# Performance work log

Measured on AMD Instinct MI355X. Metric: run time of the kernel, lower is better.

## Reference

```python
import jax, jax.numpy as jnp
import numpy as np

B, L, H, NL = 32, 1024, 4, 2
D_BERT, D_PHY, D_ACC = 1024, 7, 2
C_IN = D_BERT + D_PHY + D_ACC
D = 32
K = 20
N = B * L
E = N * K


def setup_inputs() -> dict:
    key = jax.random.key(0)
    ks = jax.random.split(key, 10)
    return {
        "protbert": jax.random.normal(ks[0], (B, 1, L, D_BERT), jnp.float32),
        "phychem": jax.random.normal(ks[1], (B, 1, L, D_PHY), jnp.float32),
        "resacc": jax.random.normal(ks[2], (B, 1, L, D_ACC), jnp.float32),
        "edge_feat": jax.random.normal(ks[3], (E, 2), jnp.float32),
        "src_idx": jax.random.randint(ks[4], (E,), 0, N, jnp.int32),
        "dst_idx": (jnp.arange(E, dtype=jnp.int32) % N),  # every node gets exactly K in-edges
        "conv_w": jax.random.normal(ks[5], (D, C_IN, 7), jnp.float32) * 0.02,
        "conv_b": jnp.zeros((D,), jnp.float32),
        "bn_gamma": jnp.ones((D,), jnp.float32),
        "bn_beta": jnp.zeros((D,), jnp.float32),
        "bn_mean": jnp.zeros((D,), jnp.float32),
        "bn_var": jnp.ones((D,), jnp.float32),
        "fc_w": jax.random.normal(ks[6], (NL, H, D, D), jnp.float32) * 0.1,
        "attn_w": jax.random.normal(ks[7], (NL, H, 2 * D + 2), jnp.float32) * 0.1,
        "fc_edge_w": jax.random.normal(ks[8], (NL, H, D, 2), jnp.float32) * 0.1,
        "fc_eatt_w": jax.random.normal(ks[9], (NL, H, 2, 2), jnp.float32) * 0.1,
    }


def _leaky(x):
    return jnp.where(x >= 0, x, 0.01 * x)


def _seg_softmax(e, dst, n):
    # softmax over incoming edges of each destination node (DGL mailbox softmax)
    m = jax.ops.segment_max(e, dst, num_segments=n)
    ex = jnp.exp(e - m[dst])
    s = jax.ops.segment_sum(ex, dst, num_segments=n)
    return ex / s[dst]


def reference(protbert, phychem, resacc, edge_feat, src_idx, dst_idx,
              conv_w, conv_b, bn_gamma, bn_beta, bn_mean, bn_var,
              fc_w, attn_w, fc_edge_w, fc_eatt_w):
    # --- Conv1d + LeakyReLU + BatchNorm1d (eval) encoder ---
    x = jnp.concatenate([protbert, phychem, resacc], axis=3)[:, 0]  # (B,L,C_IN)
    x = jnp.transpose(x, (0, 2, 1))  # (B,C_IN,L)
    x = jax.lax.conv_general_dilated(x, conv_w, (1,), [(3, 3)],
                                     dimension_numbers=("NCH", "OIH", "NCH"))
    x = _leaky(x + conv_b[None, :, None])
    scale = (bn_gamma / jnp.sqrt(bn_var + 1e-5))[None, :, None]
    x = (x - bn_mean[None, :, None]) * scale + bn_beta[None, :, None]
    feats = jnp.transpose(x, (0, 2, 1))  # (B,L,D)

    # --- stacked multi-head EGRET layers on flattened batched graph ---
    h = feats.reshape(N, D)
    alpha = None
    for l in range(NL):
        z = jnp.einsum("nd,hod->nho", h, fc_w[l])                    # (N,H,D)
        ex_t = jnp.einsum("ef,hgf->ehg", edge_feat, fc_eatt_w[l])    # (E,H,2) transformed edge feats for attn
        ez = jnp.einsum("ef,hof->eho", edge_feat, fc_edge_w[l])      # (E,H,D) edge messages
        a_src = attn_w[l][:, :D]
        a_dst = attn_w[l][:, D:2 * D]
        a_e = attn_w[l][:, 2 * D:]
        s_src = jnp.einsum("nhd,hd->nh", z, a_src)                   # node-level partial scores
        s_dst = jnp.einsum("nhd,hd->nh", z, a_dst)
        e = _leaky(s_src[src_idx] + s_dst[dst_idx]
                   + jnp.einsum("ehg,hg->eh", ex_t, a_e))            # (E,H)
        alpha = _seg_softmax(e, dst_idx, N)                          # (E,H)
        msg = alpha[:, :, None] * (z[src_idx] + ez)                  # attn on node+edge messages
        h = jax.ops.segment_sum(msg, dst_idx, num_segments=N).mean(axis=1)  # merge='avg'

    feats2 = h.reshape(B, L, D)
    out = jnp.concatenate([feats2, feats], axis=2)  # (B,L,2D)
    return out, alpha
```

## Files before the change

kernel.cpp:

```cpp
#include <hip/hip_runtime.h>
#include <hip/hip_bf16.h>
#include <cstdint>

#define B_   32
#define L_   1024
#define H_   4
#define NL_  2
#define D_   32
#define K_   20
#define N_   (B_ * L_)
#define E_   (N_ * K_)

typedef __attribute__((ext_vector_type(8))) __bf16 bf16x8;
typedef __attribute__((ext_vector_type(4))) float  f32x4;
typedef __attribute__((ext_vector_type(2))) float  f32x2;
typedef __attribute__((ext_vector_type(4))) int    i32x4;

static __device__ __forceinline__ float leaky1(float x) { return x >= 0.f ? x : 0.01f * x; }

static __device__ __forceinline__ bf16x8 cvt8(f32x4 lo, f32x4 hi) {
    bf16x8 r;
    r[0] = (__bf16)lo[0]; r[1] = (__bf16)lo[1]; r[2] = (__bf16)lo[2]; r[3] = (__bf16)lo[3];
    r[4] = (__bf16)hi[0]; r[5] = (__bf16)hi[1]; r[6] = (__bf16)hi[2]; r[7] = (__bf16)hi[3];
    return r;
}

#define GLD_LDS16(g, l) __builtin_amdgcn_global_load_lds( \
    (const __attribute__((address_space(1))) void*)(g),   \
    (__attribute__((address_space(3))) void*)(l), 16, 0, 0)

__global__ __launch_bounds__(256) void k_prep_wb(const float* __restrict__ conv_w,
                                                 __bf16* __restrict__ wb) {
    int idx = blockIdx.x * 256 + threadIdx.x;
    if (idx >= 7 * 32 * 1024) return;
    int t = idx >> 15;
    int r = idx & 32767;
    int d = r >> 10;
    int c = r & 1023;
    wb[idx] = (__bf16)conv_w[d * 7231 + c * 7 + t];
}

#define AROWS 70
__global__ __launch_bounds__(256) void k_conv_part(
    const float* __restrict__ protbert, const __bf16* __restrict__ wb,
    float* __restrict__ pbuf) {
    __shared__ __bf16 Xs[2][AROWS * 32];
    __shared__ __bf16 Bs[2][224 * 32];

    const int tid  = threadIdx.x;
    const int tok0 = blockIdx.x * 64;
    const int b    = tok0 >> 10;
    const int lb   = tok0 & 1023;
    const int cb0  = blockIdx.y * 256;

    const int row0 = tid >> 2, slot0 = tid & 3;
    const int l0 = lb + row0 - 3;
    const float* ag0 = ((unsigned)l0 < 1024u)
        ? protbert + ((size_t)b * 1024 + l0) * 1024 + cb0 + slot0 * 8 : nullptr;
    const int aoff0 = row0 * 32 + 8 * (slot0 ^ ((row0 >> 1) & 3));
    const int row1 = (256 + tid) >> 2;
    const int l1 = lb + row1 - 3;
    const float* ag1 = (tid < 24 && (unsigned)l1 < 1024u)
        ? protbert + ((size_t)b * 1024 + l1) * 1024 + cb0 + slot0 * 8 : nullptr;
    const int aoff1 = row1 * 32 + 8 * (slot0 ^ ((row1 >> 1) & 3));
    const bool has1 = (tid < 24);

    const int w    = tid >> 6;
    const int lane = tid & 63;
    const int row16 = lane & 15;
    const int kgrp  = lane >> 4;
    const int d0    = lane & 15;
    const int bslot0 = 8 * (kgrp ^ ((d0 >> 1) & 3));

    const int blrow = lane >> 2;
    const int bsl   = lane & 3;
#define STAGE_B(kc_, bf_) do {                                              \
        for (int c = w; c < 14; c += 4) {                                   \
            int brow_ = c * 16 + blrow;                                     \
            int dd_ = brow_ & 31;                                           \
            int scol_ = 8 * (bsl ^ ((dd_ >> 1) & 3));                       \
            const __bf16* gp_ = wb + (size_t)brow_ * 1024 + cb0 + (kc_) * 32 + scol_; \
            GLD_LDS16(gp_, &Bs[bf_][c * 512]);                              \
        }                                                                   \
    } while (0)

    f32x4 acc0 = {0.f, 0.f, 0.f, 0.f};
    f32x4 acc1 = {0.f, 0.f, 0.f, 0.f};

    {
        f32x4 p0l = {0,0,0,0}, p0h = {0,0,0,0}, p1l = {0,0,0,0}, p1h = {0,0,0,0};
        if (ag0) { p0l = ((const f32x4*)ag0)[0]; p0h = ((const f32x4*)ag0)[1]; }
        if (ag1) { p1l = ((const f32x4*)ag1)[0]; p1h = ((const f32x4*)ag1)[1]; }
        STAGE_B(0, 0);
        *(bf16x8*)(&Xs[0][aoff0]) = cvt8(p0l, p0h);
        if (has1) *(bf16x8*)(&Xs[0][aoff1]) = cvt8(p1l, p1h);
    }
    __syncthreads();

    int buf = 0;
    for (int kk = 0; kk < 8; ++kk) {
        f32x4 n0l = {0,0,0,0}, n0h = {0,0,0,0}, n1l = {0,0,0,0}, n1h = {0,0,0,0};
        if (kk < 7) {
            if (ag0) { n0l = ((const f32x4*)ag0)[(kk + 1) * 8]; n0h = ((const f32x4*)ag0)[(kk + 1) * 8 + 1]; }
            if (ag1) { n1l = ((const f32x4*)ag1)[(kk + 1) * 8]; n1h = ((const f32x4*)ag1)[(kk + 1) * 8 + 1]; }
            STAGE_B(kk + 1, buf ^ 1);
        }
        #pragma unroll
        for (int t = 0; t < 7; ++t) {
            int arow = w * 16 + row16 + t;
            bf16x8 a  = *(const bf16x8*)(&Xs[buf][arow * 32 + 8 * (kgrp ^ ((arow >> 1) & 3))]);
            bf16x8 b0 = *(const bf16x8*)(&Bs[buf][(t * 32 + d0) * 32 + bslot0]);
            bf16x8 b1 = *(const bf16x8*)(&Bs[buf][(t * 32 + 16 + d0) * 32 + bslot0]);
            acc0 = __builtin_amdgcn_mfma_f32_16x16x32_bf16(a, b0, acc0, 0, 0, 0);
            acc1 = __builtin_amdgcn_mfma_f32_16x16x32_bf16(a, b1, acc1, 0, 0, 0);
        }
        if (kk < 7) {
            *(bf16x8*)(&Xs[buf ^ 1][aoff0]) = cvt8(n0l, n0h);
            if (has1) *(bf16x8*)(&Xs[buf ^ 1][aoff1]) = cvt8(n1l, n1h);
        }
        __syncthreads();
        buf ^= 1;
    }

    float* pb = pbuf + ((size_t)blockIdx.y * N_ + tok0) * 32;
    #pragma unroll
    for (int i = 0; i < 4; ++i) {
        int lrow = w * 16 + kgrp * 4 + i;
        pb[lrow * 32 + d0]      = acc0[i];
        pb[lrow * 32 + 16 + d0] = acc1[i];
    }
}

__global__ __launch_bounds__(256) void k_conv_epi(
    const float* __restrict__ pbuf,     const float* __restrict__ phychem,
    const float* __restrict__ resacc,   const float* __restrict__ conv_w,
    const float* __restrict__ conv_b,   const float* __restrict__ bn_gamma,
    const float* __restrict__ bn_beta,  const float* __restrict__ bn_mean,
    const float* __restrict__ bn_var,
    float* __restrict__ feats, float* __restrict__ out) {
    __shared__ float x9[AROWS * 9];
    __shared__ float w9[9 * 7 * 32];
    __shared__ float bnA[32], bnB[32], cb[32];

    const int tid  = threadIdx.x;
    const int tok0 = blockIdx.x * 64;
    const int b    = tok0 >> 10;
    const int lb   = tok0 & 1023;

    for (int i = tid; i < 9 * 7 * 32; i += 256) {
        int d = i & 31, jt = i >> 5, t = jt % 7, j = jt / 7;
        w9[i] = conv_w[d * 7231 + (1024 + j) * 7 + t];
    }
    for (int i = tid; i < AROWS * 9; i += 256) {
        int r = i / 9, j = i % 9;
        int l = lb + r - 3;
        float v = 0.f;
        if (l >= 0 && l < L_)
            v = (j < 7) ? phychem[(b * L_ + l) * 7 + j] : resacc[(b * L_ + l) * 2 + (j - 7)];
        x9[i] = v;
    }
    if (tid < 32) {
        float sc = bn_gamma[tid] * rsqrtf(bn_var[tid] + 1e-5f);
        bnA[tid] = sc;
        bnB[tid] = bn_beta[tid] - bn_mean[tid] * sc;
        cb[tid]  = conv_b[tid];
    }
    __syncthreads();

    const int d  = tid & 31;
    const int r0 = tid >> 5;
    #pragma unroll
    for (int q = 0; q < 8; ++q) {
        int lrow = r0 * 8 + q;
        int tok  = tok0 + lrow;
        float s = pbuf[(size_t)tok * 32 + d]
                + pbuf[(size_t)(N_ + tok) * 32 + d]
                + pbuf[(size_t)(2 * N_ + tok) * 32 + d]
                + pbuf[(size_t)(3 * N_ + tok) * 32 + d];
        float c = 0.f;
        #pragma unroll
        for (int t = 0; t < 7; ++t) {
            const float* xr = &x9[(lrow + t) * 9];
            #pragma unroll
            for (int j = 0; j < 9; ++j) c += xr[j] * w9[(j * 7 + t) * 32 + d];
        }
        float v = leaky1(s + c + cb[d]) * bnA[d] + bnB[d];
        feats[(size_t)tok * 32 + d]    = v;
        out[(size_t)tok * 64 + 32 + d] = v;
    }
}

__global__ __launch_bounds__(256) void k_z(
    const float* __restrict__ hin, const float* __restrict__ fc_w,
    const float* __restrict__ attn_w, int layer,
    __bf16* __restrict__ z, float* __restrict__ ssrc, float* __restrict__ sdst) {
    __shared__ float WT[4 * 1028];
    __shared__ float As[4 * 33], Ad[4 * 33];

    const int tid = threadIdx.x;
    for (int i = tid; i < 4096; i += 256) {
        int h = i >> 10, rem = i & 1023, o = rem >> 5, d = rem & 31;
        WT[h * 1028 + d * 32 + o] = fc_w[layer * 4096 + i];
    }
    if (tid < 256) {
        int h = tid >> 6, o = tid & 63;
        float v = attn_w[layer * (4 * 66) + h * 66 + o];
        if (o < 32) As[h * 33 + o] = v; else Ad[h * 33 + (o - 32)] = v;
    }
    __syncthreads();

    const int n = blockIdx.x * 64 + (tid >> 2);
    const int h = tid & 3;

    float hrow[32];
    const f32x4* h4 = (const f32x4*)(hin + (size_t)n * 32);
    #pragma unroll
    for (int q = 0; q < 8; ++q) {
        f32x4 v = h4[q];
        hrow[q * 4 + 0] = v[0]; hrow[q * 4 + 1] = v[1];
        hrow[q * 4 + 2] = v[2]; hrow[q * 4 + 3] = v[3];
    }

    float zz[32];
    #pragma unroll
    for (int o = 0; o < 32; ++o) zz[o] = 0.f;
    #pragma unroll
    for (int d = 0; d < 32; ++d) {
        float hv = hrow[d];
        const f32x4* wt = (const f32x4*)&WT[h * 1028 + d * 32];
        #pragma unroll
        for (int o4 = 0; o4 < 8; ++o4) {
            f32x4 wv = wt[o4];
            zz[o4 * 4 + 0] += hv * wv[0]; zz[o4 * 4 + 1] += hv * wv[1];
            zz[o4 * 4 + 2] += hv * wv[2]; zz[o4 * 4 + 3] += hv * wv[3];
        }
    }
    float s1 = 0.f, s2 = 0.f;
    #pragma unroll
    for (int o = 0; o < 32; ++o) {
        s1 += zz[o] * As[h * 33 + o];
        s2 += zz[o] * Ad[h * 33 + o];
    }
    bf16x8* zo = (bf16x8*)(z + (size_t)n * 128 + h * 32);
    #pragma unroll
    for (int q = 0; q < 4; ++q) {
        bf16x8 v;
        #pragma unroll
        for (int j = 0; j < 8; ++j) v[j] = (__bf16)zz[q * 8 + j];
        zo[q] = v;
    }
    ssrc[n * 4 + h] = s1;
    sdst[n * 4 + h] = s2;
}

__global__ __launch_bounds__(256) void k_node(
    const __bf16* __restrict__ z, const float* __restrict__ ssrc,
    const float* __restrict__ sdst, const int* __restrict__ src_idx,
    const float* __restrict__ edge_feat, const float* __restrict__ attn_w,
    const float* __restrict__ fc_edge_w, const float* __restrict__ fc_eatt_w,
    int layer, float* __restrict__ hout, int hout_stride,
    float* __restrict__ alpha_out) {
    __shared__ float sWe0[4 * 32], sWe1[4 * 32];
    __shared__ float sP[4][2];
    __shared__ float sAl[4][4][24];
    __shared__ float sF[4][4][2];
    __shared__ float sEf[4][20][2];
    __shared__ int   sS[4][24];

    const int tid = threadIdx.x;
    {
        int f = tid & 1, dd = (tid >> 1) & 31, h = tid >> 6;
        float v = fc_edge_w[layer * 256 + tid];
        if (f == 0) sWe0[h * 32 + dd] = v; else sWe1[h * 32 + dd] = v;
        if (tid < 8) {
            int hh = tid >> 1, ff = tid & 1;
            float ae0 = attn_w[layer * 264 + hh * 66 + 64];
            float ae1 = attn_w[layer * 264 + hh * 66 + 65];
            float w0  = fc_eatt_w[layer * 16 + hh * 4 + 0 + ff];
            float w1  = fc_eatt_w[layer * 16 + hh * 4 + 2 + ff];
            sP[hh][ff] = ae0 * w0 + ae1 * w1;
        }
    }
    const int slot = tid >> 6, tn = tid & 63;
    const int n = blockIdx.x * 4 + slot;
    __syncthreads();

    {
        int h = tn & 3;
        float sdv = sdst[n * 4 + h];
        #pragma unroll
        for (int p = 0; p < 2; ++p) {
            int k = p * 16 + (tn >> 2);
            if (p == 0 || tn < 16) {
                int e = n + k * N_;
                int s = src_idx[e];
                f32x2 ef = *(const f32x2*)(edge_feat + (size_t)e * 2);
                float sc = ssrc[s * 4 + h] + sdv + ef.x * sP[h][0] + ef.y * sP[h][1];
                sAl[slot][h][k] = leaky1(sc);
                if (h == 0) { sS[slot][k] = s; sEf[slot][k][0] = ef.x; sEf[slot][k][1] = ef.y; }
            }
        }
    }
    __syncthreads();

    if (tn < 4) {
        int h = tn;
        float m = -1e30f;
        for (int k = 0; k < 20; ++k) m = fmaxf(m, sAl[slot][h][k]);
        float ssum = 0.f;
        for (int k = 0; k < 20; ++k) {
            float v = __expf(sAl[slot][h][k] - m);
            sAl[slot][h][k] = v;
            ssum += v;
        }
        float inv = 1.f / ssum;
        float F0 = 0.f, F1 = 0.f;
        for (int k = 0; k < 20; ++k) {
            float a = sAl[slot][h][k] * inv;
            sAl[slot][h][k] = a;
            F0 += a * sEf[slot][k][0];
            F1 += a * sEf[slot][k][1];
        }
        sF[slot][h][0] = F0;
        sF[slot][h][1] = F1;
    }
    __syncthreads();

    if (alpha_out != nullptr) {
        #pragma unroll
        for (int p = 0; p < 2; ++p) {
            int k = p * 16 + (tn >> 2), h = tn & 3;
            if (p == 0 || tn < 16)
                alpha_out[(size_t)(n + k * N_) * 4 + h] = sAl[slot][h][k];
        }
    }

    {
        const int h = tn >> 4, dp = tn & 15;
        f32x4 areg[5];
        i32x4 sreg[5];
        #pragma unroll
        for (int q = 0; q < 5; ++q) {
            areg[q] = *(const f32x4*)(&sAl[slot][h][q * 4]);
            sreg[q] = *(const i32x4*)(&sS[slot][q * 4]);
        }
        float F0 = sF[slot][h][0], F1 = sF[slot][h][1];
        float w0a = sWe0[h * 32 + dp * 2], w0b = sWe0[h * 32 + dp * 2 + 1];
        float w1a = sWe1[h * 32 + dp * 2], w1b = sWe1[h * 32 + dp * 2 + 1];
        float acca = F0 * w0a + F1 * w1a;
        float accb = F0 * w0b + F1 * w1b;
        #pragma unroll
        for (int k = 0; k < 20; ++k) {
            int sk = __builtin_amdgcn_readfirstlane(sreg[k >> 2][k & 3]);
            const uint32_t* zp = (const uint32_t*)(z + (size_t)sk * 128);
            uint32_t u = zp[tn];
            float zl = __uint_as_float(u << 16);
            float zh = __uint_as_float(u & 0xffff0000u);
            float a = areg[k >> 2][k & 3];
            acca = fmaf(a, zl, acca);
            accb = fmaf(a, zh, accb);
        }
        acca += __shfl_xor(acca, 16); acca += __shfl_xor(acca, 32);
        accb += __shfl_xor(accb, 16); accb += __shfl_xor(accb, 32);
        if (tn < 16) {
            f32x2 o = {0.25f * acca, 0.25f * accb};
            *(f32x2*)(hout + (size_t)n * hout_stride + dp * 2) = o;
        }
    }
}

extern "C" void kernel_launch(void* const* d_in, const int* in_sizes, int n_in,
                              void* d_out, int out_size, void* d_ws, size_t ws_size,
                              hipStream_t stream) {
    const float* protbert  = (const float*)d_in[0];
    const float* phychem   = (const float*)d_in[1];
    const float* resacc    = (const float*)d_in[2];
    const float* edge_feat = (const float*)d_in[3];
    const int*   src_idx   = (const int*)d_in[4];
    const float* conv_w    = (const float*)d_in[6];
    const float* conv_b    = (const float*)d_in[7];
    const float* bn_gamma  = (const float*)d_in[8];
    const float* bn_beta   = (const float*)d_in[9];
    const float* bn_mean   = (const float*)d_in[10];
    const float* bn_var    = (const float*)d_in[11];
    const float* fc_w      = (const float*)d_in[12];
    const float* attn_w    = (const float*)d_in[13];
    const float* fc_edge_w = (const float*)d_in[14];
    const float* fc_eatt_w = (const float*)d_in[15];

    char* ws = (char*)d_ws;
    __bf16* wb   = (__bf16*)(ws);
    float* feats = (float*)(ws + (1u  << 20));
    float* h1    = (float*)(ws + (5u  << 20));
    float* ssrc  = (float*)(ws + (9u  << 20));
    float* sdst  = (float*)(ws + (10u << 20));
    __bf16* z    = (__bf16*)(ws + (11u << 20));
    float* pbuf  = (float*)(ws + (24u << 20));

    float* out       = (float*)d_out;
    float* alpha_out = out + (size_t)N_ * 64;

    k_prep_wb<<<896, 256, 0, stream>>>(conv_w, wb);
    k_conv_part<<<dim3(512, 4), 256, 0, stream>>>(protbert, wb, pbuf);
    k_conv_epi<<<512, 256, 0, stream>>>(pbuf, phychem, resacc, conv_w, conv_b,
                                        bn_gamma, bn_beta, bn_mean, bn_var, feats, out);
    k_z<<<512, 256, 0, stream>>>(feats, fc_w, attn_w, 0, z, ssrc, sdst);
    k_node<<<N_ / 4, 256, 0, stream>>>(z, ssrc, sdst, src_idx, edge_feat, attn_w,
                                       fc_edge_w, fc_eatt_w, 0, h1, 32, nullptr);
    k_z<<<512, 256, 0, stream>>>(h1, fc_w, attn_w, 1, z, ssrc, sdst);
    k_node<<<N_ / 4, 256, 0, stream>>>(z, ssrc, sdst, src_idx, edge_feat, attn_w,
                                       fc_edge_w, fc_eatt_w, 1, out, 64, alpha_out);
}
```

Baseline: 151.6 us.

## Double conv tile rows per block and fuse conv epilogue with layer-0 projection

Result: faster. 138.8 us (-8.5%).

```diff
diff --git a/kernel.cpp b/kernel.cpp
--- a/kernel.cpp
+++ b/kernel.cpp
@@ -40,33 +40,37 @@
     wb[idx] = (__bf16)conv_w[d * 7231 + c * 7 + t];
 }
 
-#define AROWS 70
+#define XR2 134
 __global__ __launch_bounds__(256) void k_conv_part(
     const float* __restrict__ protbert, const __bf16* __restrict__ wb,
     float* __restrict__ pbuf) {
-    __shared__ __bf16 Xs[2][AROWS * 32];
+    __shared__ __bf16 Xs[2][XR2 * 32];
     __shared__ __bf16 Bs[2][224 * 32];
 
     const int tid  = threadIdx.x;
-    const int tok0 = blockIdx.x * 64;
+    const int tok0 = blockIdx.x * 128;
     const int b    = tok0 >> 10;
     const int lb   = tok0 & 1023;
     const int cb0  = blockIdx.y * 256;
 
-    const int row0 = tid >> 2, slot0 = tid & 3;
-    const int l0 = lb + row0 - 3;
+    const int slot0 = tid & 3;
+    const int row0 = tid >> 2;
+    const int row1 = 64 + (tid >> 2);
+    const int row2 = 128 + (tid >> 2);
+    const int l0 = lb + row0 - 3, l1 = lb + row1 - 3, l2 = lb + row2 - 3;
     const float* ag0 = ((unsigned)l0 < 1024u)
         ? protbert + ((size_t)b * 1024 + l0) * 1024 + cb0 + slot0 * 8 : nullptr;
+    const float* ag1 = ((unsigned)l1 < 1024u)
+        ? protbert + ((size_t)b * 1024 + l1) * 1024 + cb0 + slot0 * 8 : nullptr;
+    const bool has2 = (tid < 24);
+    const float* ag2 = (has2 && (unsigned)l2 < 1024u)
+        ? protbert + ((size_t)b * 1024 + l2) * 1024 + cb0 + slot0 * 8 : nullptr;
     const int aoff0 = row0 * 32 + 8 * (slot0 ^ ((row0 >> 1) & 3));
-    const int row1 = (256 + tid) >> 2;
-    const int l1 = lb + row1 - 3;
-    const float* ag1 = (tid < 24 && (unsigned)l1 < 1024u)
-        ? protbert + ((size_t)b * 1024 + l1) * 1024 + cb0 + slot0 * 8 : nullptr;
     const int aoff1 = row1 * 32 + 8 * (slot0 ^ ((row1 >> 1) & 3));
-    const bool has1 = (tid < 24);
-
-    const int w    = tid >> 6;
-    const int lane = tid & 63;
+    const int aoff2 = row2 * 32 + 8 * (slot0 ^ ((row2 >> 1) & 3));
+
+    const int w     = tid >> 6;
+    const int lane  = tid & 63;
     const int row16 = lane & 15;
     const int kgrp  = lane >> 4;
     const int d0    = lane & 15;
@@ -84,39 +88,49 @@
         }                                                                   \
     } while (0)
 
-    f32x4 acc0 = {0.f, 0.f, 0.f, 0.f};
-    f32x4 acc1 = {0.f, 0.f, 0.f, 0.f};
+    f32x4 acc[2][2];
+    acc[0][0] = (f32x4){0,0,0,0}; acc[0][1] = (f32x4){0,0,0,0};
+    acc[1][0] = (f32x4){0,0,0,0}; acc[1][1] = (f32x4){0,0,0,0};
 
     {
         f32x4 p0l = {0,0,0,0}, p0h = {0,0,0,0}, p1l = {0,0,0,0}, p1h = {0,0,0,0};
+        f32x4 p2l = {0,0,0,0}, p2h = {0,0,0,0};
         if (ag0) { p0l = ((const f32x4*)ag0)[0]; p0h = ((const f32x4*)ag0)[1]; }
         if (ag1) { p1l = ((const f32x4*)ag1)[0]; p1h = ((const f32x4*)ag1)[1]; }
+        if (ag2) { p2l = ((const f32x4*)ag2)[0]; p2h = ((const f32x4*)ag2)[1]; }
         STAGE_B(0, 0);
         *(bf16x8*)(&Xs[0][aoff0]) = cvt8(p0l, p0h);
-        if (has1) *(bf16x8*)(&Xs[0][aoff1]) = cvt8(p1l, p1h);
+        *(bf16x8*)(&Xs[0][aoff1]) = cvt8(p1l, p1h);
+        if (has2) *(bf16x8*)(&Xs[0][aoff2]) = cvt8(p2l, p2h);
     }
     __syncthreads();
 
     int buf = 0;
     for (int kk = 0; kk < 8; ++kk) {
         f32x4 n0l = {0,0,0,0}, n0h = {0,0,0,0}, n1l = {0,0,0,0}, n1h = {0,0,0,0};
+        f32x4 n2l = {0,0,0,0}, n2h = {0,0,0,0};
         if (kk < 7) {
             if (ag0) { n0l = ((const f32x4*)ag0)[(kk + 1) * 8]; n0h = ((const f32x4*)ag0)[(kk + 1) * 8 + 1]; }
             if (ag1) { n1l = ((const f32x4*)ag1)[(kk + 1) * 8]; n1h = ((const f32x4*)ag1)[(kk + 1) * 8 + 1]; }
+            if (ag2) { n2l = ((const f32x4*)ag2)[(kk + 1) * 8]; n2h = ((const f32x4*)ag2)[(kk + 1) * 8 + 1]; }
             STAGE_B(kk + 1, buf ^ 1);
         }
         #pragma unroll
         for (int t = 0; t < 7; ++t) {
-            int arow = w * 16 + row16 + t;
-            bf16x8 a  = *(const bf16x8*)(&Xs[buf][arow * 32 + 8 * (kgrp ^ ((arow >> 1) & 3))]);
             bf16x8 b0 = *(const bf16x8*)(&Bs[buf][(t * 32 + d0) * 32 + bslot0]);
             bf16x8 b1 = *(const bf16x8*)(&Bs[buf][(t * 32 + 16 + d0) * 32 + bslot0]);
-            acc0 = __builtin_amdgcn_mfma_f32_16x16x32_bf16(a, b0, acc0, 0, 0, 0);
-            acc1 = __builtin_amdgcn_mfma_f32_16x16x32_bf16(a, b1, acc1, 0, 0, 0);
+            #pragma unroll
+            for (int mt = 0; mt < 2; ++mt) {
+                int arow = w * 32 + mt * 16 + row16 + t;
+                bf16x8 a = *(const bf16x8*)(&Xs[buf][arow * 32 + 8 * (kgrp ^ ((arow >> 1) & 3))]);
+                acc[mt][0] = __builtin_amdgcn_mfma_f32_16x16x32_bf16(a, b0, acc[mt][0], 0, 0, 0);
+                acc[mt][1] = __builtin_amdgcn_mfma_f32_16x16x32_bf16(a, b1, acc[mt][1], 0, 0, 0);
+            }
         }
         if (kk < 7) {
             *(bf16x8*)(&Xs[buf ^ 1][aoff0]) = cvt8(n0l, n0h);
-            if (has1) *(bf16x8*)(&Xs[buf ^ 1][aoff1]) = cvt8(n1l, n1h);
+            *(bf16x8*)(&Xs[buf ^ 1][aoff1]) = cvt8(n1l, n1h);
+            if (has2) *(bf16x8*)(&Xs[buf ^ 1][aoff2]) = cvt8(n2l, n2h);
         }
         __syncthreads();
         buf ^= 1;
@@ -124,29 +138,46 @@
 
     float* pb = pbuf + ((size_t)blockIdx.y * N_ + tok0) * 32;
     #pragma unroll
-    for (int i = 0; i < 4; ++i) {
-        int lrow = w * 16 + kgrp * 4 + i;
-        pb[lrow * 32 + d0]      = acc0[i];
-        pb[lrow * 32 + 16 + d0] = acc1[i];
-    }
-}
-
-__global__ __launch_bounds__(256) void k_conv_epi(
+    for (int mt = 0; mt < 2; ++mt)
+        #pragma unroll
+        for (int i = 0; i < 4; ++i) {
+            int lrow = w * 32 + mt * 16 + kgrp * 4 + i;
+            pb[lrow * 32 + d0]      = acc[mt][0][i];
+            pb[lrow * 32 + 16 + d0] = acc[mt][1][i];
+        }
+}
+
+#define AROWS 70
+__global__ __launch_bounds__(256) void k_epi_z0(
     const float* __restrict__ pbuf,     const float* __restrict__ phychem,
     const float* __restrict__ resacc,   const float* __restrict__ conv_w,
     const float* __restrict__ conv_b,   const float* __restrict__ bn_gamma,
     const float* __restrict__ bn_beta,  const float* __restrict__ bn_mean,
-    const float* __restrict__ bn_var,
-    float* __restrict__ feats, float* __restrict__ out) {
+    const float* __restrict__ bn_var,   const float* __restrict__ fc_w,
+    const float* __restrict__ attn_w,
+    float* __restrict__ out, __bf16* __restrict__ z,
+    float* __restrict__ ssrc, float* __restrict__ sdst) {
+    __shared__ float WT[4 * 1028];
+    __shared__ float As[4 * 33], Ad[4 * 33];
     __shared__ float x9[AROWS * 9];
     __shared__ float w9[9 * 7 * 32];
     __shared__ float bnA[32], bnB[32], cb[32];
+    __shared__ float fs[64 * 36];
 
     const int tid  = threadIdx.x;
     const int tok0 = blockIdx.x * 64;
     const int b    = tok0 >> 10;
     const int lb   = tok0 & 1023;
 
+    for (int i = tid; i < 4096; i += 256) {
+        int h = i >> 10, rem = i & 1023, o = rem >> 5, d = rem & 31;
+        WT[h * 1028 + d * 32 + o] = fc_w[i];
+    }
+    {
+        int h = tid >> 6, o = tid & 63;
+        float v = attn_w[h * 66 + o];
+        if (o < 32) As[h * 33 + o] = v; else Ad[h * 33 + (o - 32)] = v;
+    }
     for (int i = tid; i < 9 * 7 * 32; i += 256) {
         int d = i & 31, jt = i >> 5, t = jt % 7, j = jt / 7;
         w9[i] = conv_w[d * 7231 + (1024 + j) * 7 + t];
@@ -155,8 +186,8 @@
         int r = i / 9, j = i % 9;
         int l = lb + r - 3;
         float v = 0.f;
-        if (l >= 0 && l < L_)
-            v = (j < 7) ? phychem[(b * L_ + l) * 7 + j] : resacc[(b * L_ + l) * 2 + (j - 7)];
+        if ((unsigned)l < 1024u)
+            v = (j < 7) ? phychem[(b * 1024 + l) * 7 + j] : resacc[(b * 1024 + l) * 2 + (j - 7)];
         x9[i] = v;
     }
     if (tid < 32) {
@@ -167,26 +198,74 @@
     }
     __syncthreads();
 
-    const int d  = tid & 31;
-    const int r0 = tid >> 5;
-    #pragma unroll
-    for (int q = 0; q < 8; ++q) {
-        int lrow = r0 * 8 + q;
-        int tok  = tok0 + lrow;
-        float s = pbuf[(size_t)tok * 32 + d]
-                + pbuf[(size_t)(N_ + tok) * 32 + d]
-                + pbuf[(size_t)(2 * N_ + tok) * 32 + d]
-                + pbuf[(size_t)(3 * N_ + tok) * 32 + d];
-        float c = 0.f;
-        #pragma unroll
-        for (int t = 0; t < 7; ++t) {
-            const float* xr = &x9[(lrow + t) * 9];
+    {
+        const int d  = tid & 31;
+        const int r0 = tid >> 5;
+        #pragma unroll
+        for (int q = 0; q < 8; ++q) {
+            int lrow = r0 * 8 + q;
+            int tok  = tok0 + lrow;
+            float s = pbuf[(size_t)tok * 32 + d]
+                    + pbuf[(size_t)(N_ + tok) * 32 + d]
+                    + pbuf[(size_t)(2 * N_ + tok) * 32 + d]
+                    + pbuf[(size_t)(3 * N_ + tok) * 32 + d];
+            float c = 0.f;
             #pragma unroll
-            for (int j = 0; j < 9; ++j) c += xr[j] * w9[(j * 7 + t) * 32 + d];
-        }
-        float v = leaky1(s + c + cb[d]) * bnA[d] + bnB[d];
-        feats[(size_t)tok * 32 + d]    = v;
-        out[(size_t)tok * 64 + 32 + d] = v;
+            for (int t = 0; t < 7; ++t) {
+                const float* xr = &x9[(lrow + t) * 9];
+                #pragma unroll
+                for (int j = 0; j < 9; ++j) c += xr[j] * w9[(j * 7 + t) * 32 + d];
+            }
+            float v = leaky1(s + c + cb[d]) * bnA[d] + bnB[d];
+            out[(size_t)tok * 64 + 32 + d] = v;
+            fs[lrow * 36 + d] = v;
+        }
+    }
+    __syncthreads();
+
+    {
+        const int nl = tid >> 2;
+        const int h  = tid & 3;
+        const int n  = tok0 + nl;
+
+        float hrow[32];
+        const f32x4* h4 = (const f32x4*)(&fs[nl * 36]);
+        #pragma unroll
+        for (int q = 0; q < 8; ++q) {
+            f32x4 v = h4[q];
+            hrow[q * 4 + 0] = v[0]; hrow[q * 4 + 1] = v[1];
+            hrow[q * 4 + 2] = v[2]; hrow[q * 4 + 3] = v[3];
+        }
+        float zz[32];
+        #pragma unroll
+        for (int o = 0; o < 32; ++o) zz[o] = 0.f;
+        #pragma unroll
+        for (int d = 0; d < 32; ++d) {
+            float hv = hrow[d];
+            const f32x4* wt = (const f32x4*)&WT[h * 1028 + d * 32];
+            #pragma unroll
+            for (int o4 = 0; o4 < 8; ++o4) {
+                f32x4 wv = wt[o4];
+                zz[o4 * 4 + 0] += hv * wv[0]; zz[o4 * 4 + 1] += hv * wv[1];
+                zz[o4 * 4 + 2] += hv * wv[2]; zz[o4 * 4 + 3] += hv * wv[3];
+            }
+        }
+        float s1 = 0.f, s2 = 0.f;
+        #pragma unroll
+        for (int o = 0; o < 32; ++o) {
+            s1 += zz[o] * As[h * 33 + o];
+            s2 += zz[o] * Ad[h * 33 + o];
+        }
+        bf16x8* zo = (bf16x8*)(z + (size_t)n * 128 + h * 32);
+        #pragma unroll
+        for (int q = 0; q < 4; ++q) {
+            bf16x8 v;
+            #pragma unroll
+            for (int j = 0; j < 8; ++j) v[j] = (__bf16)zz[q * 8 + j];
+            zo[q] = v;
+        }
+        ssrc[n * 4 + h] = s1;
+        sdst[n * 4 + h] = s2;
     }
 }
 
@@ -202,7 +281,7 @@
         int h = i >> 10, rem = i & 1023, o = rem >> 5, d = rem & 31;
         WT[h * 1028 + d * 32 + o] = fc_w[layer * 4096 + i];
     }
-    if (tid < 256) {
+    {
         int h = tid >> 6, o = tid & 63;
         float v = attn_w[layer * (4 * 66) + h * 66 + o];
         if (o < 32) As[h * 33 + o] = v; else Ad[h * 33 + (o - 32)] = v;
@@ -390,7 +469,6 @@
 
     char* ws = (char*)d_ws;
     __bf16* wb   = (__bf16*)(ws);
-    float* feats = (float*)(ws + (1u  << 20));
     float* h1    = (float*)(ws + (5u  << 20));
     float* ssrc  = (float*)(ws + (9u  << 20));
     float* sdst  = (float*)(ws + (10u << 20));
@@ -401,10 +479,10 @@
     float* alpha_out = out + (size_t)N_ * 64;
 
     k_prep_wb<<<896, 256, 0, stream>>>(conv_w, wb);
-    k_conv_part<<<dim3(512, 4), 256, 0, stream>>>(protbert, wb, pbuf);
-    k_conv_epi<<<512, 256, 0, stream>>>(pbuf, phychem, resacc, conv_w, conv_b,
-                                        bn_gamma, bn_beta, bn_mean, bn_var, feats, out);
-    k_z<<<512, 256, 0, stream>>>(feats, fc_w, attn_w, 0, z, ssrc, sdst);
+    k_conv_part<<<dim3(256, 4), 256, 0, stream>>>(protbert, wb, pbuf);
+    k_epi_z0<<<512, 256, 0, stream>>>(pbuf, phychem, resacc, conv_w, conv_b,
+                                      bn_gamma, bn_beta, bn_mean, bn_var,
+                                      fc_w, attn_w, out, z, ssrc, sdst);
     k_node<<<N_ / 4, 256, 0, stream>>>(z, ssrc, sdst, src_idx, edge_feat, attn_w,
                                        fc_edge_w, fc_eatt_w, 0, h1, 32, nullptr);
     k_z<<<512, 256, 0, stream>>>(h1, fc_w, attn_w, 1, z, ssrc, sdst);
```
